# Kernel optimization log

Hardware: AMD Instinct MI355X
Metric: run time of the kernel (lower is better)

The kernel has to match this reference:

```python
import jax, jax.numpy as jnp
import numpy as np

BS, TS, NA, OS = 32, 256, 16, 512
HID, D, W = 1024, 128, 8            # sw_hidden_dim, sw_input_dim, sw_window_size
OUT, DEC, NACT = 512, 512, 30       # sw_output_dim, sw_decoder_hidden_layer, n_actions


def setup_inputs() -> dict:
    key = jax.random.key(0)
    ks = jax.random.split(key, 12)
    p = lambda k, shape: jax.random.normal(k, shape, jnp.float32) * 0.02
    return {
        "inputs": jax.random.normal(ks[0], (BS, TS, NA, OS), jnp.float32),
        "hidden_state": jnp.zeros((BS, NA, (W - 1) * D), jnp.float32),
        "w1": p(ks[1], (OS, HID)),        "b1": jnp.zeros((HID,), jnp.float32),
        "w2": p(ks[2], (HID, D)),         "b2": jnp.zeros((D,), jnp.float32),
        "w3": p(ks[3], (W * D, OUT)),     "b3": jnp.zeros((OUT,), jnp.float32),
        "w4": p(ks[4], (OUT, DEC)),       "b4": jnp.zeros((DEC,), jnp.float32),
        "w5": p(ks[5], (DEC, NACT)),      "b5": jnp.zeros((NACT,), jnp.float32),
    }


def reference(inputs, hidden_state, w1, b1, w2, b2, w3, b3, w4, b4, w5, b5):
    bs, ts, na, _ = inputs.shape
    # encoder: two pointwise MLP layers over (bs, ts, na, *)
    x = jax.nn.relu(inputs @ w1 + b1)          # (bs, ts, na, HID)
    x = jax.nn.relu(x @ w2 + b2)               # (bs, ts, na, D)
    # build the full frame sequence: W-1 hidden frames followed by ts encoded frames
    hid_frames = hidden_state.reshape(bs, na, W - 1, D)
    seq = jnp.concatenate([hid_frames, jnp.transpose(x, (0, 2, 1, 3))], axis=2)  # (bs, na, ts+W-1, D)
    # sliding windows: window at step t = frames [t, t+W) — vectorized over all t
    wins = jnp.stack([seq[:, :, i:i + ts, :] for i in range(W)], axis=3)  # (bs, na, ts, W, D)
    wins = wins.reshape(bs, na, ts, W * D)
    h = jax.nn.relu(wins @ w3 + b3)            # (bs, na, ts, OUT)
    h = jnp.transpose(h, (0, 2, 1, 3))         # (bs, ts, na, OUT)
    h = jax.nn.relu(h @ w4 + b4)               # (bs, ts, na, DEC)
    q = h @ w5 + b5                            # (bs, ts, na, NACT)
    # final carried window: last W-1 frames of the sequence, flattened per agent
    window = seq[:, :, ts:, :].reshape(bs, na, (W - 1) * D)
    return (q, window)
```

## Files before the change

### kernel.cpp

```cpp
#include <hip/hip_runtime.h>
#include <hip/hip_bf16.h>
#include <hip/hip_fp8.h>


#define DEVI __device__ __forceinline__

typedef float f32x4 __attribute__((ext_vector_type(4)));
typedef short s16x8 __attribute__((ext_vector_type(8)));
typedef short s16x4 __attribute__((ext_vector_type(4)));
typedef long long i64;
typedef unsigned long long u64;

#define ROWS 131072
#define SEQ_T 263

#define W2P_OFF 524288
#define W5P_OFF 1441792

#define W3P8_BYTE_OFF 2916352
#define SEQ8_BYTE_OFF 3440640
#define W4P8_BYTE_OFF 20971520
#define BIG_BYTE_OFF 37388288

DEVI short f2bf(float f) {
  union { __hip_bfloat16 h; short s; } u;
  u.h = __float2bfloat16(f);
  return u.s;
}
DEVI float bf2f(short s) {
  union { float f; unsigned int u; } v;
  v.u = ((unsigned int)(unsigned short)s) << 16;
  return v.f;
}

DEVI unsigned int f2e4(float f) {
  union { __hip_fp8_e4m3 h; unsigned char c; } u;
  u.h = __hip_fp8_e4m3(f);
  return (unsigned int)u.c;
}

#if __has_builtin(__builtin_amdgcn_cvt_pk_fp8_f32)
DEVI unsigned int pk4e4(float a, float b, float c, float d) {
  int v = 0;
  v = __builtin_amdgcn_cvt_pk_fp8_f32(a, b, v, false);
  v = __builtin_amdgcn_cvt_pk_fp8_f32(c, d, v, true);
  return (unsigned int)v;
}
#else
DEVI unsigned int pk4e4(float a, float b, float c, float d) {
  return f2e4(a) | (f2e4(b) << 8) | (f2e4(c) << 16) | (f2e4(d) << 24);
}
#endif

DEVI f32x4 MFMA(s16x8 a, s16x8 b, f32x4 c) {
  return __builtin_amdgcn_mfma_f32_16x16x32_bf16(a, b, c, 0, 0, 0);
}
DEVI f32x4 MFMA8(i64 a, i64 b, f32x4 c) {
  return __builtin_amdgcn_mfma_f32_16x16x32_fp8_fp8(a, b, c, 0, 0, 0);
}

__global__ __launch_bounds__(256) void prep_kernel(
    const float* __restrict__ w1, const float* __restrict__ w2,
    const float* __restrict__ w3, const float* __restrict__ w4,
    const float* __restrict__ w5, const float* __restrict__ hid,
    short* __restrict__ wp, unsigned char* __restrict__ wp8,
    unsigned char* __restrict__ w3p8, unsigned char* __restrict__ w4p8,
    unsigned char* __restrict__ seq8)
{
  int t0 = blockIdx.x * 256 + threadIdx.x;
  if (t0 < 671744) {
    int idx = t0;
    const float* src; int sh, Nsrc, local; long dsto;
    if (idx < W2P_OFF)     { src = w1; sh = 4; Nsrc = 1024; local = idx;           dsto = idx; }
    else if (idx < 655360) { src = w2; sh = 5; Nsrc = 128;  local = idx - W2P_OFF; dsto = idx; }
    else                   { src = w5; sh = 4; Nsrc = 30;   local = idx - 655360;  dsto = W5P_OFF + (idx - 655360); }
    int j    = local & 7;
    int lane = (local >> 3) & 63;
    int rest = local >> 9;
    int k0   = rest & ((1 << sh) - 1);
    int n0   = rest >> sh;
    int k = (k0 << 5) + ((lane >> 4) << 3) + j;
    int n = (n0 << 4) + (lane & 15);
    float v = (n < Nsrc) ? src[k * Nsrc + n] : 0.f;
    wp[dsto] = f2bf(v);
  } else if (t0 < 851968) {
    int t = t0 - 671744;
    const float* src; int nkshift, Nsrc, dt; unsigned char* dst;
    if (t < 65536)       { src = w1; dt = t;          nkshift = 4; Nsrc = 1024; dst = wp8; }
    else if (t < 81920)  { src = w2; dt = t - 65536;  nkshift = 5; Nsrc = 128;  dst = wp8 + 524288; }
    else if (t < 147456) { src = w3; dt = t - 81920;  nkshift = 5; Nsrc = 512;  dst = w3p8; }
    else                 { src = w4; dt = t - 147456; nkshift = 4; Nsrc = 512;  dst = w4p8; }
    int lane = dt & 63;
    int rest = dt >> 6;
    int k0   = rest & ((1 << nkshift) - 1);
    int n0   = rest >> nkshift;
    int kb = (k0 << 5) + ((lane >> 4) << 3);
    int n  = (n0 << 4) + (lane & 15);
    float v[8];
    #pragma unroll
    for (int j = 0; j < 8; ++j) v[j] = src[(kb + j) * Nsrc + n];
    u64 pk = (u64)pk4e4(v[0], v[1], v[2], v[3])
           | ((u64)pk4e4(v[4], v[5], v[6], v[7]) << 32);
    *(u64*)(dst + (long)dt * 8) = pk;
  } else {
    int t = t0 - 851968;
    int j = t & 15;
    int r = t >> 4;
    int i = r % 7;
    int ba = r / 7;
    int s = j ^ i;
    const float* src = hid + (r << 7) + (j << 3);
    f32x4 a = *(const f32x4*)src;
    f32x4 b = *(const f32x4*)(src + 4);
    u64 pk = (u64)pk4e4(a[0], a[1], a[2], a[3])
           | ((u64)pk4e4(b[0], b[1], b[2], b[3]) << 32);
    *(u64*)(seq8 + (ba * SEQ_T + i) * 128 + s * 8) = pk;
  }
}

__global__ __launch_bounds__(512, 4) void enc_kernel(
    const float* __restrict__ inp, const unsigned char* __restrict__ w1p8,
    const float* __restrict__ b1, const unsigned char* __restrict__ w2p8,
    const float* __restrict__ b2, unsigned char* __restrict__ seq8)
{
  __shared__ unsigned char As8[32768] __attribute__((aligned(16)));
  __shared__ unsigned char h1q8[32768] __attribute__((aligned(16)));
  const int tid = threadIdx.x;
  const int lane = tid & 63, wv = tid >> 6;
  const int l15 = lane & 15, lg = lane >> 4;
  const int rb = blockIdx.x << 6;

  #pragma unroll
  for (int it = 0; it < 8; ++it) {
    int g = it * 512 + tid;
    int row = g >> 6, j = g & 63;
    const float* s = inp + (long)(rb + row) * 512 + j * 8;
    f32x4 v0 = *(const f32x4*)s;
    f32x4 v1 = *(const f32x4*)(s + 4);
    u64 pk = (u64)pk4e4(v0[0], v0[1], v0[2], v0[3])
           | ((u64)pk4e4(v1[0], v1[1], v1[2], v1[3]) << 32);
    *(u64*)(As8 + (j << 9) + ((row ^ (j & 15)) << 3)) = pk;
  }
  __syncthreads();

  f32x4 z = {0.f, 0.f, 0.f, 0.f};
  f32x4 acc2[4] = {z, z, z, z};

  for (int p = 0; p < 2; ++p) {
    f32x4 acc1[4][4];
    #pragma unroll
    for (int i = 0; i < 4; ++i)
      #pragma unroll
      for (int j = 0; j < 4; ++j) acc1[i][j] = z;

    const unsigned char* wB = w1p8 + (((p * 32 + wv * 4) * 16) << 9) + lane * 8;

    i64 Wc[4];
    #pragma unroll
    for (int ci = 0; ci < 4; ++ci) Wc[ci] = *(const i64*)(wB + ((ci * 16) << 9));

    #pragma unroll 1
    for (int k0 = 0; k0 < 16; ++k0) {
      int kn = (k0 + 1) & 15;
      i64 Wn[4];
      #pragma unroll
      for (int ci = 0; ci < 4; ++ci) Wn[ci] = *(const i64*)(wB + ((ci * 16 + kn) << 9));
      int k2 = k0 * 4 + lg;
      int c = k2 & 15;
      i64 Xc[4];
      #pragma unroll
      for (int mi = 0; mi < 4; ++mi)
        Xc[mi] = *(const i64*)(As8 + (k2 << 9) + (((mi * 16 + l15) ^ c) << 3));
      #pragma unroll
      for (int ci = 0; ci < 4; ++ci)
        #pragma unroll
        for (int mi = 0; mi < 4; ++mi)
          acc1[ci][mi] = MFMA8(Wc[ci], Xc[mi], acc1[ci][mi]);
      #pragma unroll
      for (int ci = 0; ci < 4; ++ci) Wc[ci] = Wn[ci];
    }
    __syncthreads();
    #pragma unroll
    for (int ci = 0; ci < 4; ++ci) {
      f32x4 bv = *(const f32x4*)(b1 + p * 512 + wv * 64 + ci * 16 + lg * 4);
      int k2c = wv * 8 + ci * 2 + (lg >> 1);
      int half = (lg & 1) << 2;
      #pragma unroll
      for (int mi = 0; mi < 4; ++mi) {
        int m = mi * 16 + l15;
        unsigned int pk = pk4e4(fmaxf(acc1[ci][mi][0] + bv[0], 0.f),
                                fmaxf(acc1[ci][mi][1] + bv[1], 0.f),
                                fmaxf(acc1[ci][mi][2] + bv[2], 0.f),
                                fmaxf(acc1[ci][mi][3] + bv[3], 0.f));
        *(unsigned int*)(h1q8 + (k2c << 9) + (m << 3) + half) = pk;
      }
    }
    __syncthreads();
    const unsigned char* w2B = w2p8 + ((wv * 32 + p * 16) << 9) + lane * 8;
    i64 W2c = *(const i64*)(w2B);
    #pragma unroll 1
    for (int kk = 0; kk < 16; ++kk) {
      int kn = (kk + 1) & 15;
      i64 W2n = *(const i64*)(w2B + (kn << 9));
      i64 X2[4];
      #pragma unroll
      for (int mi = 0; mi < 4; ++mi)
        X2[mi] = *(const i64*)(h1q8 + ((kk * 4 + lg) << 9) + ((mi * 16 + l15) << 3));
      #pragma unroll
      for (int mi = 0; mi < 4; ++mi)
        acc2[mi] = MFMA8(W2c, X2[mi], acc2[mi]);
      W2c = W2n;
    }
  }
  __syncthreads();
  unsigned char* scr8 = As8;
  {
    f32x4 bv = *(const f32x4*)(b2 + wv * 16 + lg * 4);
    int gsb = wv * 2 + (lg >> 1);
    int off4 = (lg & 1) << 2;
    #pragma unroll
    for (int mi = 0; mi < 4; ++mi) {
      int m = mi * 16 + l15;
      int f15 = ((rb >> 4) + mi + 7) & 15;
      unsigned int pk = pk4e4(fmaxf(acc2[mi][0] + bv[0], 0.f),
                              fmaxf(acc2[mi][1] + bv[1], 0.f),
                              fmaxf(acc2[mi][2] + bv[2], 0.f),
                              fmaxf(acc2[mi][3] + bv[3], 0.f));
      int ls = (gsb ^ f15) ^ (m & 15);
      *(unsigned int*)(scr8 + m * 128 + ls * 8 + off4) = pk;
    }
  }
  __syncthreads();
  #pragma unroll
  for (int it = 0; it < 2; ++it) {
    int c = it * 512 + tid;
    int i = c >> 4, s = c & 15;
    u64 v = *(const u64*)(scr8 + i * 128 + ((s ^ (i & 15)) << 3));
    int r = rb + i;
    int ba2 = ((r >> 12) << 4) + (r & 15);
    int t = (r >> 4) & 255;
    int f = t + 7;
    *(u64*)(seq8 + (ba2 * SEQ_T + f) * 128 + (s << 3)) = v;
  }
}

__global__ __launch_bounds__(256) void enc_hi_kernel(
    const float* __restrict__ inp, const short* __restrict__ w1p,
    const float* __restrict__ b1, const short* __restrict__ w2p,
    const float* __restrict__ b2, float* __restrict__ out)
{
  __shared__ short As[8192]  __attribute__((aligned(16)));
  __shared__ short h1s[16384] __attribute__((aligned(16)));
  const int tid = threadIdx.x;
  const int lane = tid & 63, wv = tid >> 6;
  const int l15 = lane & 15, lg = lane >> 4;
  const int b = blockIdx.x / 7, ti = blockIdx.x % 7;
  const int t = 249 + ti;
  const long row0 = (long)b * 4096 + t * 16;

  #pragma unroll
  for (int it = 0; it < 4; ++it) {
    int c = it * 256 + tid;
    int m = c >> 6, j = c & 63;
    const float* s = inp + (row0 + m) * 512 + j * 8;
    f32x4 v0 = *(const f32x4*)s;
    f32x4 v1 = *(const f32x4*)(s + 4);
    s16x8 o;
    o[0]=f2bf(v0[0]); o[1]=f2bf(v0[1]); o[2]=f2bf(v0[2]); o[3]=f2bf(v0[3]);
    o[4]=f2bf(v1[0]); o[5]=f2bf(v1[1]); o[6]=f2bf(v1[2]); o[7]=f2bf(v1[3]);
    *(s16x8*)((char*)As + (j << 8) + (((m ^ (j & 15)) & 15) << 4)) = o;
  }
  __syncthreads();

  f32x4 z = {0.f, 0.f, 0.f, 0.f};
  f32x4 acc1[16];
  #pragma unroll
  for (int i = 0; i < 16; ++i) acc1[i] = z;
  #pragma unroll 1
  for (int k0 = 0; k0 < 16; ++k0) {
    int k2 = k0 * 4 + lg;
    s16x8 X = *(const s16x8*)((const char*)As + (k2 << 8) + (((l15 ^ (k2 & 15)) & 15) << 4));
    #pragma unroll
    for (int ci = 0; ci < 16; ++ci) {
      s16x8 W = *(const s16x8*)(w1p + (((wv * 16 + ci) * 16 + k0) << 9) + lane * 8);
      acc1[ci] = MFMA(W, X, acc1[ci]);
    }
  }
  #pragma unroll
  for (int ci = 0; ci < 16; ++ci) {
    f32x4 bv = *(const f32x4*)(b1 + wv * 256 + ci * 16 + lg * 4);
    int k2c = wv * 32 + ci * 2 + (lg >> 1);
    int half = (lg & 1) << 3;
    s16x4 o;
    #pragma unroll
    for (int j = 0; j < 4; ++j)
      o[j] = f2bf(fmaxf(acc1[ci][j] + bv[j], 0.f));
    *(s16x4*)((char*)h1s + (k2c << 8) + (l15 << 4) + half) = o;
  }
  __syncthreads();
  f32x4 acc2[2] = {z, z};
  #pragma unroll 1
  for (int kk = 0; kk < 32; ++kk) {
    s16x8 X2 = *(const s16x8*)((const char*)h1s + ((kk * 4 + lg) << 8) + (l15 << 4));
    #pragma unroll
    for (int nf = 0; nf < 2; ++nf) {
      s16x8 W2 = *(const s16x8*)(w2p + (((wv * 2 + nf) * 32 + kk) << 9) + lane * 8);
      acc2[nf] = MFMA(W2, X2, acc2[nf]);
    }
  }
  #pragma unroll
  for (int nf = 0; nf < 2; ++nf) {
    #pragma unroll
    for (int rr = 0; rr < 4; ++rr) {
      int d = (wv * 2 + nf) * 16 + lg * 4 + rr;
      float v = fmaxf(acc2[nf][rr] + b2[d], 0.f);
      out[3932160 + (((b * 16 + l15) * 7 + ti) << 7) + d] = v;
    }
  }
}

__global__ __launch_bounds__(512, 4) void win_kernel(
    const unsigned char* __restrict__ seq8, const unsigned char* __restrict__ w3p8,
    const float* __restrict__ b3, unsigned char* __restrict__ h3p8)
{
  __shared__ unsigned char sh8[17280] __attribute__((aligned(16)));
  __shared__ short rp[8192] __attribute__((aligned(16)));
  const int tid = threadIdx.x;
  const int lane = tid & 63, wid = tid >> 6;
  const int wm = wid >> 2, wn = wid & 3;
  const int l15 = lane & 15, lg = lane >> 4;
  const int bid = blockIdx.x;
  const int th = bid & 1, ba = bid >> 1;
  const int t0 = th << 7;

  const unsigned char* gsrc = seq8 + (ba * SEQ_T + t0) * 128;
  #pragma unroll
  for (int i = 0; i < 3; ++i) {
    int c = i * 512 + tid;
    if (c < 1080) *(s16x8*)&sh8[c * 16] = *(const s16x8*)(gsrc + c * 16);
  }
  __syncthreads();

  f32x4 z = {0.f, 0.f, 0.f, 0.f};
  for (int h = 0; h < 2; ++h) {
    f32x4 acc[4][4];
    #pragma unroll
    for (int i = 0; i < 4; ++i)
      #pragma unroll
      for (int j = 0; j < 4; ++j) acc[i][j] = z;

    const unsigned char* bB = w3p8 + (((h * 16 + wn * 4) * 32) << 9) + lane * 8;
    i64 bcur[4];
    #pragma unroll
    for (int nf = 0; nf < 4; ++nf) bcur[nf] = *(const i64*)(bB + ((nf * 32) << 9));

    #pragma unroll 1
    for (int kc = 0; kc < 32; ++kc) {
      int kn = (kc + 1) & 31;
      i64 bnxt[4];
      #pragma unroll
      for (int nf = 0; nf < 4; ++nf) bnxt[nf] = *(const i64*)(bB + ((nf * 32 + kn) << 9));
      int w = kc >> 2;
      int dslot = ((kc & 3) << 2) + lg;
      i64 av[4];
      #pragma unroll
      for (int mf = 0; mf < 4; ++mf) {
        int f = wm * 64 + mf * 16 + l15 + w;
        av[mf] = *(const i64*)(sh8 + f * 128 + ((dslot ^ (f & 15)) << 3));
      }
      #pragma unroll
      for (int nf = 0; nf < 4; ++nf)
        #pragma unroll
        for (int mf = 0; mf < 4; ++mf)
          acc[mf][nf] = MFMA8(av[mf], bcur[nf], acc[mf][nf]);
      #pragma unroll
      for (int nf = 0; nf < 4; ++nf) bcur[nf] = bnxt[nf];
    }

    for (int s = 0; s < 4; ++s) {
      __syncthreads();
      #pragma unroll
      for (int mf = 0; mf < 4; ++mf) {
        float bias = b3[h * 256 + wn * 64 + s * 16 + l15];
        int lc = wn * 16 + l15;
        #pragma unroll
        for (int rr = 0; rr < 4; ++rr) {
          int row = wm * 64 + mf * 16 + lg * 4 + rr;
          float v = fmaxf(acc[mf][s][rr] + bias, 0.f);
          int by = ((row << 7) + (lc << 1)) ^ ((row & 7) << 4);
          rp[by >> 1] = f2bf(v);
        }
      }
      __syncthreads();
      #pragma unroll
      for (int it = 0; it < 2; ++it) {
        int c = it * 512 + tid;
        int cl = c & 15, qh = (c >> 4) & 1, wnl = (c >> 5) & 3, tt = (c >> 7) & 7;
        int row = tt * 16 + cl;
        int qb = wnl * 16 + qh * 8;
        int by = ((row << 7) + (qb << 1)) ^ ((row & 7) << 4);
        s16x8 v = *(const s16x8*)((const char*)rp + by);
        u64 pk = (u64)pk4e4(bf2f(v[0]), bf2f(v[1]), bf2f(v[2]), bf2f(v[3]))
               | ((u64)pk4e4(bf2f(v[4]), bf2f(v[5]), bf2f(v[6]), bf2f(v[7])) << 32);
        int k0g = h * 8 + wnl * 2 + (s >> 1);
        int g = ((s & 1) << 1) + qh;
        int mt = ba * 16 + th * 8 + tt;
        long dst = ((long)((mt * 16 + k0g) * 64 + g * 16 + cl)) << 3;
        *(u64*)(h3p8 + dst) = pk;
      }
    }
  }
}

__global__ __launch_bounds__(512, 4) void dec_kernel(
    const unsigned char* __restrict__ h3p8, const unsigned char* __restrict__ w4p8,
    const float* __restrict__ b4, const short* __restrict__ w5p,
    const float* __restrict__ b5, float* __restrict__ out)
{
  __shared__ short h4s[32768] __attribute__((aligned(16)));
  const int tid = threadIdx.x;
  const int lane = tid & 63, wid = tid >> 6;
  const int wm = wid >> 2, wn = wid & 3;
  const int mf5 = wid;
  const int l15 = lane & 15, lg = lane >> 4;
  const int rb = blockIdx.x << 7;

  f32x4 z = {0.f, 0.f, 0.f, 0.f};
  f32x4 acc5[2] = {z, z};
  const unsigned char* aBase = h3p8 + (long)((rb >> 4) + wm * 4) * 8192 + lane * 8;

  for (int h = 0; h < 2; ++h) {
    f32x4 acc[4][4];
    #pragma unroll
    for (int i = 0; i < 4; ++i)
      #pragma unroll
      for (int j = 0; j < 4; ++j) acc[i][j] = z;

    const unsigned char* bB = w4p8 + (((h * 16 + wn * 4) * 16) << 9) + lane * 8;
    i64 bcur[4];
    #pragma unroll
    for (int nf = 0; nf < 4; ++nf) bcur[nf] = *(const i64*)(bB + ((nf * 16) << 9));

    #pragma unroll 1
    for (int k0 = 0; k0 < 16; ++k0) {
      int kn = (k0 + 1) & 15;
      i64 bnxt[4];
      #pragma unroll
      for (int nf = 0; nf < 4; ++nf) bnxt[nf] = *(const i64*)(bB + ((nf * 16 + kn) << 9));
      i64 av[4];
      #pragma unroll
      for (int mf = 0; mf < 4; ++mf) av[mf] = *(const i64*)(aBase + mf * 8192 + k0 * 512);
      #pragma unroll
      for (int nf = 0; nf < 4; ++nf)
        #pragma unroll
        for (int mf = 0; mf < 4; ++mf)
          acc[mf][nf] = MFMA8(av[mf], bcur[nf], acc[mf][nf]);
      #pragma unroll
      for (int nf = 0; nf < 4; ++nf) bcur[nf] = bnxt[nf];
    }
    __syncthreads();
    #pragma unroll
    for (int mf = 0; mf < 4; ++mf)
      #pragma unroll
      for (int nf = 0; nf < 4; ++nf) {
        int lc = wn * 64 + nf * 16 + l15;
        float bias = b4[h * 256 + lc];
        #pragma unroll
        for (int rr = 0; rr < 4; ++rr) {
          int row = wm * 64 + mf * 16 + lg * 4 + rr;
          float v = fmaxf(acc[mf][nf][rr] + bias, 0.f);
          int by = ((row << 9) + (lc << 1)) ^ ((row & 7) << 4);
          h4s[by >> 1] = f2bf(v);
        }
      }
    __syncthreads();
    #pragma unroll
    for (int kk = 0; kk < 8; ++kk) {
      int row = mf5 * 16 + l15;
      int by = ((row << 9) + (kk << 6) + (lg << 4)) ^ ((row & 7) << 4);
      s16x8 a0 = *(const s16x8*)((const char*)h4s + by);
      #pragma unroll
      for (int nf = 0; nf < 2; ++nf) {
        s16x8 wb = *(const s16x8*)(w5p + (nf * 16 + h * 8 + kk) * 512 + lane * 8);
        acc5[nf] = MFMA(a0, wb, acc5[nf]);
      }
    }
  }
  #pragma unroll
  for (int nf = 0; nf < 2; ++nf) {
    int col = nf * 16 + l15;
    if (col < 30) {
      float bias = b5[col];
      #pragma unroll
      for (int rr = 0; rr < 4; ++rr) {
        int row_ = rb + mf5 * 16 + lg * 4 + rr;
        int t = row_ & 255;
        int ba2 = row_ >> 8;
        int orow = (((ba2 >> 4) << 8) + t) * 16 + (ba2 & 15);
        out[orow * 30 + col] = acc5[nf][rr] + bias;
      }
    }
  }
}

extern "C" void kernel_launch(void* const* d_in, const int* in_sizes, int n_in,
                              void* d_out, int out_size, void* d_ws, size_t ws_size,
                              hipStream_t stream) {
  const float* inp = (const float*)d_in[0];
  const float* hid = (const float*)d_in[1];
  const float* w1  = (const float*)d_in[2];
  const float* b1  = (const float*)d_in[3];
  const float* w2  = (const float*)d_in[4];
  const float* b2  = (const float*)d_in[5];
  const float* w3  = (const float*)d_in[6];
  const float* b3  = (const float*)d_in[7];
  const float* w4  = (const float*)d_in[8];
  const float* b4  = (const float*)d_in[9];
  const float* w5  = (const float*)d_in[10];
  const float* b5  = (const float*)d_in[11];

  char* ws = (char*)d_ws;
  short* wp   = (short*)ws;
  short* w1p  = wp;
  short* w2p  = wp + W2P_OFF;
  short* w5p  = wp + W5P_OFF;
  unsigned char* w3p8 = (unsigned char*)(ws + W3P8_BYTE_OFF);
  unsigned char* seq8 = (unsigned char*)(ws + SEQ8_BYTE_OFF);
  unsigned char* w4p8 = (unsigned char*)(ws + W4P8_BYTE_OFF);
  unsigned char* h3p8 = (unsigned char*)(ws + BIG_BYTE_OFF);
  unsigned char* w1p8 = h3p8;
  unsigned char* w2p8 = w1p8 + 524288;
  float* out  = (float*)d_out;

  prep_kernel   <<<3552, 256, 0, stream>>>(w1, w2, w3, w4, w5, hid,
                                           wp, w1p8, w3p8, w4p8, seq8);
  enc_kernel    <<<2048, 512, 0, stream>>>(inp, w1p8, b1, w2p8, b2, seq8);
  enc_hi_kernel <<<224, 256, 0, stream>>>(inp, w1p, b1, w2p, b2, out);
  win_kernel    <<<1024, 512, 0, stream>>>(seq8, w3p8, b3, h3p8);
  dec_kernel    <<<1024, 512, 0, stream>>>(h3p8, w4p8, b4, w5p, b5, out);
}
```

Baseline: 389.2 us.

## Fold high-precision tail encoder into main encoder launch and swizzle LDS tiles

```diff
diff --git a/kernel.cpp b/kernel.cpp
--- a/kernel.cpp
+++ b/kernel.cpp
@@ -121,14 +121,81 @@
 __global__ __launch_bounds__(512, 4) void enc_kernel(
     const float* __restrict__ inp, const unsigned char* __restrict__ w1p8,
     const float* __restrict__ b1, const unsigned char* __restrict__ w2p8,
-    const float* __restrict__ b2, unsigned char* __restrict__ seq8)
+    const float* __restrict__ b2, unsigned char* __restrict__ seq8,
+    const short* __restrict__ w1p, const short* __restrict__ w2p,
+    float* __restrict__ out)
 {
-  __shared__ unsigned char As8[32768] __attribute__((aligned(16)));
-  __shared__ unsigned char h1q8[32768] __attribute__((aligned(16)));
+  __shared__ char smem[65536] __attribute__((aligned(16)));
   const int tid = threadIdx.x;
   const int lane = tid & 63, wv = tid >> 6;
   const int l15 = lane & 15, lg = lane >> 4;
-  const int rb = blockIdx.x << 6;
+  f32x4 z = {0.f, 0.f, 0.f, 0.f};
+
+  if (blockIdx.x < 224) {
+    short* As  = (short*)smem;
+    short* h1s = (short*)(smem + 16384);
+    const int b = blockIdx.x / 7, ti = blockIdx.x % 7;
+    const int t = 249 + ti;
+    const long row0 = (long)b * 4096 + t * 16;
+
+    #pragma unroll
+    for (int it = 0; it < 2; ++it) {
+      int c = it * 512 + tid;
+      int m = c >> 6, j = c & 63;
+      const float* s = inp + (row0 + m) * 512 + j * 8;
+      f32x4 v0 = *(const f32x4*)s;
+      f32x4 v1 = *(const f32x4*)(s + 4);
+      s16x8 o;
+      o[0]=f2bf(v0[0]); o[1]=f2bf(v0[1]); o[2]=f2bf(v0[2]); o[3]=f2bf(v0[3]);
+      o[4]=f2bf(v1[0]); o[5]=f2bf(v1[1]); o[6]=f2bf(v1[2]); o[7]=f2bf(v1[3]);
+      *(s16x8*)((char*)As + (j << 8) + (((m ^ (j & 15)) & 15) << 4)) = o;
+    }
+    __syncthreads();
+
+    f32x4 acc1[8];
+    #pragma unroll
+    for (int i = 0; i < 8; ++i) acc1[i] = z;
+    #pragma unroll 1
+    for (int k0 = 0; k0 < 16; ++k0) {
+      int k2 = k0 * 4 + lg;
+      s16x8 X = *(const s16x8*)((const char*)As + (k2 << 8) + (((l15 ^ (k2 & 15)) & 15) << 4));
+      #pragma unroll
+      for (int ci = 0; ci < 8; ++ci) {
+        s16x8 W = *(const s16x8*)(w1p + (((wv * 8 + ci) * 16 + k0) << 9) + lane * 8);
+        acc1[ci] = MFMA(W, X, acc1[ci]);
+      }
+    }
+    #pragma unroll
+    for (int ci = 0; ci < 8; ++ci) {
+      f32x4 bv = *(const f32x4*)(b1 + wv * 128 + ci * 16 + lg * 4);
+      int k2c = wv * 16 + ci * 2 + (lg >> 1);
+      int half = (lg & 1) << 3;
+      s16x4 o;
+      #pragma unroll
+      for (int j = 0; j < 4; ++j)
+        o[j] = f2bf(fmaxf(acc1[ci][j] + bv[j], 0.f));
+      *(s16x4*)((char*)h1s + (k2c << 8) + (l15 << 4) + half) = o;
+    }
+    __syncthreads();
+    f32x4 acc2 = z;
+    #pragma unroll 1
+    for (int kk = 0; kk < 32; ++kk) {
+      s16x8 X2 = *(const s16x8*)((const char*)h1s + ((kk * 4 + lg) << 8) + (l15 << 4));
+      s16x8 W2 = *(const s16x8*)(w2p + (((wv * 32 + kk)) << 9) + lane * 8);
+      acc2 = MFMA(W2, X2, acc2);
+    }
+    #pragma unroll
+    for (int rr = 0; rr < 4; ++rr) {
+      int d = wv * 16 + lg * 4 + rr;
+      float v = fmaxf(acc2[rr] + b2[d], 0.f);
+      out[3932160 + (((b * 16 + l15) * 7 + ti) << 7) + d] = v;
+    }
+    return;
+  }
+
+  unsigned char* As8  = (unsigned char*)smem;
+  unsigned char* h1q8 = (unsigned char*)(smem + 32768);
+  const int rb = (blockIdx.x - 224) << 6;
 
   #pragma unroll
   for (int it = 0; it < 8; ++it) {
@@ -143,7 +210,6 @@
   }
   __syncthreads();
 
-  f32x4 z = {0.f, 0.f, 0.f, 0.f};
   f32x4 acc2[4] = {z, z, z, z};
 
   for (int p = 0; p < 2; ++p) {
@@ -192,7 +258,7 @@
                                 fmaxf(acc1[ci][mi][1] + bv[1], 0.f),
                                 fmaxf(acc1[ci][mi][2] + bv[2], 0.f),
                                 fmaxf(acc1[ci][mi][3] + bv[3], 0.f));
-        *(unsigned int*)(h1q8 + (k2c << 9) + (m << 3) + half) = pk;
+        *(unsigned int*)(h1q8 + (k2c << 9) + ((m ^ (k2c & 15)) << 3) + half) = pk;
       }
     }
     __syncthreads();
@@ -202,10 +268,11 @@
     for (int kk = 0; kk < 16; ++kk) {
       int kn = (kk + 1) & 15;
       i64 W2n = *(const i64*)(w2B + (kn << 9));
+      int row = kk * 4 + lg;
       i64 X2[4];
       #pragma unroll
       for (int mi = 0; mi < 4; ++mi)
-        X2[mi] = *(const i64*)(h1q8 + ((kk * 4 + lg) << 9) + ((mi * 16 + l15) << 3));
+        X2[mi] = *(const i64*)(h1q8 + (row << 9) + (((mi * 16 + l15) ^ (row & 15)) << 3));
       #pragma unroll
       for (int mi = 0; mi < 4; ++mi)
         acc2[mi] = MFMA8(W2c, X2[mi], acc2[mi]);
@@ -241,81 +308,6 @@
     int t = (r >> 4) & 255;
     int f = t + 7;
     *(u64*)(seq8 + (ba2 * SEQ_T + f) * 128 + (s << 3)) = v;
-  }
-}
-
-__global__ __launch_bounds__(256) void enc_hi_kernel(
-    const float* __restrict__ inp, const short* __restrict__ w1p,
-    const float* __restrict__ b1, const short* __restrict__ w2p,
-    const float* __restrict__ b2, float* __restrict__ out)
-{
-  __shared__ short As[8192]  __attribute__((aligned(16)));
-  __shared__ short h1s[16384] __attribute__((aligned(16)));
-  const int tid = threadIdx.x;
-  const int lane = tid & 63, wv = tid >> 6;
-  const int l15 = lane & 15, lg = lane >> 4;
-  const int b = blockIdx.x / 7, ti = blockIdx.x % 7;
-  const int t = 249 + ti;
-  const long row0 = (long)b * 4096 + t * 16;
-
-  #pragma unroll
-  for (int it = 0; it < 4; ++it) {
-    int c = it * 256 + tid;
-    int m = c >> 6, j = c & 63;
-    const float* s = inp + (row0 + m) * 512 + j * 8;
-    f32x4 v0 = *(const f32x4*)s;
-    f32x4 v1 = *(const f32x4*)(s + 4);
-    s16x8 o;
-    o[0]=f2bf(v0[0]); o[1]=f2bf(v0[1]); o[2]=f2bf(v0[2]); o[3]=f2bf(v0[3]);
-    o[4]=f2bf(v1[0]); o[5]=f2bf(v1[1]); o[6]=f2bf(v1[2]); o[7]=f2bf(v1[3]);
-    *(s16x8*)((char*)As + (j << 8) + (((m ^ (j & 15)) & 15) << 4)) = o;
-  }
-  __syncthreads();
-
-  f32x4 z = {0.f, 0.f, 0.f, 0.f};
-  f32x4 acc1[16];
-  #pragma unroll
-  for (int i = 0; i < 16; ++i) acc1[i] = z;
-  #pragma unroll 1
-  for (int k0 = 0; k0 < 16; ++k0) {
-    int k2 = k0 * 4 + lg;
-    s16x8 X = *(const s16x8*)((const char*)As + (k2 << 8) + (((l15 ^ (k2 & 15)) & 15) << 4));
-    #pragma unroll
-    for (int ci = 0; ci < 16; ++ci) {
-      s16x8 W = *(const s16x8*)(w1p + (((wv * 16 + ci) * 16 + k0) << 9) + lane * 8);
-      acc1[ci] = MFMA(W, X, acc1[ci]);
-    }
-  }
-  #pragma unroll
-  for (int ci = 0; ci < 16; ++ci) {
-    f32x4 bv = *(const f32x4*)(b1 + wv * 256 + ci * 16 + lg * 4);
-    int k2c = wv * 32 + ci * 2 + (lg >> 1);
-    int half = (lg & 1) << 3;
-    s16x4 o;
-    #pragma unroll
-    for (int j = 0; j < 4; ++j)
-      o[j] = f2bf(fmaxf(acc1[ci][j] + bv[j], 0.f));
-    *(s16x4*)((char*)h1s + (k2c << 8) + (l15 << 4) + half) = o;
-  }
-  __syncthreads();
-  f32x4 acc2[2] = {z, z};
-  #pragma unroll 1
-  for (int kk = 0; kk < 32; ++kk) {
-    s16x8 X2 = *(const s16x8*)((const char*)h1s + ((kk * 4 + lg) << 8) + (l15 << 4));
-    #pragma unroll
-    for (int nf = 0; nf < 2; ++nf) {
-      s16x8 W2 = *(const s16x8*)(w2p + (((wv * 2 + nf) * 32 + kk) << 9) + lane * 8);
-      acc2[nf] = MFMA(W2, X2, acc2[nf]);
-    }
-  }
-  #pragma unroll
-  for (int nf = 0; nf < 2; ++nf) {
-    #pragma unroll
-    for (int rr = 0; rr < 4; ++rr) {
-      int d = (wv * 2 + nf) * 16 + lg * 4 + rr;
-      float v = fmaxf(acc2[nf][rr] + b2[d], 0.f);
-      out[3932160 + (((b * 16 + l15) * 7 + ti) << 7) + d] = v;
-    }
   }
 }
 
@@ -469,7 +461,7 @@
         for (int rr = 0; rr < 4; ++rr) {
           int row = wm * 64 + mf * 16 + lg * 4 + rr;
           float v = fmaxf(acc[mf][nf][rr] + bias, 0.f);
-          int by = ((row << 9) + (lc << 1)) ^ ((row & 7) << 4);
+          int by = ((row << 9) + (lc << 1)) ^ ((row & 15) << 4);
           h4s[by >> 1] = f2bf(v);
         }
       }
@@ -477,7 +469,7 @@
     #pragma unroll
     for (int kk = 0; kk < 8; ++kk) {
       int row = mf5 * 16 + l15;
-      int by = ((row << 9) + (kk << 6) + (lg << 4)) ^ ((row & 7) << 4);
+      int by = ((row << 9) + (kk << 6) + (lg << 4)) ^ ((row & 15) << 4);
       s16x8 a0 = *(const s16x8*)((const char*)h4s + by);
       #pragma unroll
       for (int nf = 0; nf < 2; ++nf) {
@@ -532,10 +524,10 @@
   unsigned char* w2p8 = w1p8 + 524288;
   float* out  = (float*)d_out;
 
-  prep_kernel   <<<3552, 256, 0, stream>>>(w1, w2, w3, w4, w5, hid,
-                                           wp, w1p8, w3p8, w4p8, seq8);
-  enc_kernel    <<<2048, 512, 0, stream>>>(inp, w1p8, b1, w2p8, b2, seq8);
-  enc_hi_kernel <<<224, 256, 0, stream>>>(inp, w1p, b1, w2p, b2, out);
-  win_kernel    <<<1024, 512, 0, stream>>>(seq8, w3p8, b3, h3p8);
-  dec_kernel    <<<1024, 512, 0, stream>>>(h3p8, w4p8, b4, w5p, b5, out);
-}
+  prep_kernel <<<3552, 256, 0, stream>>>(w1, w2, w3, w4, w5, hid,
+                                         wp, w1p8, w3p8, w4p8, seq8);
+  enc_kernel  <<<2272, 512, 0, stream>>>(inp, w1p8, b1, w2p8, b2, seq8,
+                                         w1p, w2p, out);
+  win_kernel  <<<1024, 512, 0, stream>>>(seq8, w3p8, b3, h3p8);
+  dec_kernel  <<<1024, 512, 0, stream>>>(h3p8, w4p8, b4, w5p, b5, out);
+}
```

Result: no change. 392.8 us (+0.9%).
